# Optimization experiments

Hardware: AMD Instinct MI355X
Metric: run time of the kernel (lower is better)

The kernel has to match this reference:

```python
import jax, jax.numpy as jnp
import numpy as np

# ctlib options layout: [views, dets, width, height, dImg, dDet, Ang0, dAng, s2r, d2r, binshift]
VIEWS = 512
DETS = 512
H_IMG = 256
W_IMG = 256
D_IMG = 0.006641
D_DET = 0.0072
ANG0 = 0.0
D_ANG = 2.0 * np.pi / VIEWS
S2R = 5.95
D2R = 4.906
VIRDET = D_DET * S2R / (S2R + D2R)  # virtual detector spacing at isocenter


def make_filter():
    # ramp (Ram-Lak) filter in spatial domain, length 2*dets-1
    x = np.arange(2 * DETS - 1) - DETS + 1
    x2 = np.where(x == 0, 1, x * x).astype(np.float64)
    f = np.where(np.abs(x) % 2 == 1, -1.0 / (np.pi ** 2 * x2 * VIRDET ** 2), 0.0)
    f = np.where(x == 0, 1.0 / (4.0 * VIRDET ** 2), f)
    return jnp.asarray(f, dtype=jnp.float32).reshape(1, 1, 1, -1)


def make_w():
    # cosine (distance) pre-weight * quadrature step (virdet * pi / views)
    u = (np.arange(DETS) - DETS / 2 + 0.5) * VIRDET
    w = S2R / np.sqrt(S2R ** 2 + u ** 2) * VIRDET * np.pi / VIEWS
    return jnp.asarray(w, dtype=jnp.float32).reshape(1, 1, 1, -1)


def setup_inputs() -> dict:
    key = jax.random.key(0)
    projection = jax.random.normal(key, (2, 1, VIEWS, DETS), dtype=jnp.float32)
    return {"projection": projection, "w": make_w(), "filt": make_filter()}


def ramp_filter(p, filt):
    # p: [B,1,V,D], filt: [1,1,1,2D-1] -> [B,1,V,D] (same padding along detector axis)
    return jax.lax.conv_general_dilated(
        p, filt, window_strides=(1, 1),
        padding=((0, 0), (DETS - 1, DETS - 1)),
        dimension_numbers=("NCHW", "OIHW", "NCHW"))


def backproject_sv(p):
    # pixel-driven equidistant fan-beam backprojection, one output channel per view
    # p: [B,1,V,D] -> [B,V,H,W]
    p3 = p[:, 0]  # [B,V,D]
    betas = ANG0 + D_ANG * jnp.arange(VIEWS, dtype=jnp.float32)
    cb = jnp.cos(betas)[:, None, None]  # [V,1,1]
    sb = jnp.sin(betas)[:, None, None]
    xs = ((jnp.arange(W_IMG, dtype=jnp.float32) - (W_IMG - 1) / 2.0) * D_IMG)[None, None, :]
    ys = (((H_IMG - 1) / 2.0 - jnp.arange(H_IMG, dtype=jnp.float32)) * D_IMG)[None, :, None]
    d = S2R - (xs * cb + ys * sb)               # [V,H,W] source-to-pixel depth
    u = S2R * (ys * cb - xs * sb) / d           # virtual-detector coordinate
    wgt = (S2R / d) ** 2                        # fan-beam U^{-2} weight
    t = u / VIRDET + (DETS - 1) / 2.0           # fractional detector index
    i0 = jnp.floor(t).astype(jnp.int32)
    frac = t - i0
    v0 = (i0 >= 0) & (i0 < DETS)
    v1 = (i0 + 1 >= 0) & (i0 + 1 < DETS)
    i0c = jnp.clip(i0, 0, DETS - 1)
    i1c = jnp.clip(i0 + 1, 0, DETS - 1)
    gather = jax.vmap(lambda pv, idx: pv[:, idx], in_axes=(1, 0), out_axes=1)
    vals0 = gather(p3, i0c)  # [B,V,H,W]
    vals1 = gather(p3, i1c)
    w0 = ((1.0 - frac) * v0)[None]
    w1 = (frac * v1)[None]
    return wgt[None] * (vals0 * w0 + vals1 * w1)


def reference(projection, w, filt):
    p = projection * w                 # per-detector ramp pre-weight
    p = ramp_filter(p, filt)           # full-width ramp convolution
    return backproject_sv(p)           # per-view backprojection [B,V,H,W]
```

## Files before the change

### kernel.cpp

```cpp
#include <hip/hip_runtime.h>
#include <math.h>

#define VIEWS 512
#define DETS  512

typedef float f32x4 __attribute__((ext_vector_type(4)));
typedef float f32x2 __attribute__((ext_vector_type(2)));

constexpr double S2R_D    = 5.95;
constexpr double D2R_D    = 4.906;
constexpr double DDET_D   = 0.0072;
constexpr double VIRDET_D = DDET_D * S2R_D / (S2R_D + D2R_D);
constexpr double DANG_D   = 2.0 * 3.14159265358979323846 / (double)VIEWS;
constexpr double DIMG_D   = 0.006641;

__global__ __launch_bounds__(512, 4) void fbp_fused_kernel(
    const float* __restrict__ proj, const float* __restrict__ wq,
    const float* __restrict__ filt, float* __restrict__ out)
{
    __shared__ __align__(16) float pwpad[2][1536];
    __shared__ __align__(16) float sfe[520];
    __shared__ __align__(16) float rows01[1536];

    const int tid = threadIdx.x;
    const int v   = blockIdx.x;

    const float beta = (float)DANG_D * (float)v;
    const float cb = cosf(beta);
    const float sb = sinf(beta);

    {
        const f32x4 z = {0.f, 0.f, 0.f, 0.f};
        f32x4* pz = (f32x4*)&pwpad[0][0];
        pz[tid] = z;
        if (tid < 256) pz[512 + tid] = z;
        f32x4* rz = (f32x4*)rows01;
        if (tid < 384) rz[tid] = z;
        for (int i = tid; i < 520; i += 512)
            sfe[i] = (i < 512) ? filt[2*i] : 0.0f;
    }
    __syncthreads();

    if (tid < 256) {
        const int rl  = tid >> 7;
        const int t2  = tid & 127;
        const int row = rl * VIEWS + v;
        const f32x4 p4 = *(const f32x4*)(proj + ((size_t)row << 9) + 4*t2);
        const f32x4 w4 = *(const f32x4*)(wq + 4*t2);
        pwpad[rl][511 + 4*t2 + 0] = p4.x * w4.x;
        pwpad[rl][511 + 4*t2 + 1] = p4.y * w4.y;
        pwpad[rl][511 + 4*t2 + 2] = p4.z * w4.z;
        pwpad[rl][511 + 4*t2 + 3] = p4.w * w4.w;
    }
    __syncthreads();

    const int lane = tid & 63;
    const int warp = tid >> 6;

    if (warp < 4) {
        const int rl2 = warp >> 1;
        const int wv  = warp & 1;
        const int d0  = 256*wv + 4*lane;
        const float* P = &pwpad[rl2][0];
        const int e_lo = wv ? 0 : 124;
        const int G    = wv ? 48 : 49;
        const float c0 = filt[511];
        float a0=0.f, a1=0.f, a2=0.f, a3=0.f;
        for (int g = 0; g < G; ++g) {
            const int e0 = e_lo + 8*g;
            const f32x4 S0 = *(const f32x4*)&sfe[e0];
            const f32x4 S1 = *(const f32x4*)&sfe[e0 + 4];
            const float* Pb = P + d0 + 2*e0;
            const f32x4 q0 = *(const f32x4*)(Pb + 0);
            const f32x4 q1 = *(const f32x4*)(Pb + 4);
            const f32x4 q2 = *(const f32x4*)(Pb + 8);
            const f32x4 q3 = *(const f32x4*)(Pb + 12);
            const f32x4 q4 = *(const f32x4*)(Pb + 16);
            const float p[20] = {q0.x,q0.y,q0.z,q0.w, q1.x,q1.y,q1.z,q1.w,
                                 q2.x,q2.y,q2.z,q2.w, q3.x,q3.y,q3.z,q3.w,
                                 q4.x,q4.y,q4.z,q4.w};
            const float s[8]  = {S0.x,S0.y,S0.z,S0.w, S1.x,S1.y,S1.z,S1.w};
            #pragma unroll
            for (int j = 0; j < 8; ++j) {
                a0 = fmaf(p[2*j + 0], s[j], a0);
                a1 = fmaf(p[2*j + 1], s[j], a1);
                a2 = fmaf(p[2*j + 2], s[j], a2);
                a3 = fmaf(p[2*j + 3], s[j], a3);
            }
        }
        a0 = fmaf(P[511 + d0 + 0], c0, a0);
        a1 = fmaf(P[511 + d0 + 1], c0, a1);
        a2 = fmaf(P[511 + d0 + 2], c0, a2);
        a3 = fmaf(P[511 + d0 + 3], c0, a3);
        float* W = &rows01[((128 + d0) << 1) + rl2];
        W[0] = a0; W[2] = a1; W[4] = a2; W[6] = a3;
    }
    __syncthreads();

    {
        const float D    = (float)DIMG_D;
        const float Kf   = (float)(S2R_D / VIRDET_D);
        const int   xi   = 4*lane;
        const float xs0  = ((float)xi - 127.5f) * D;
        const float xc0  = xs0 * cb;
        const float xsbK = (xs0 * sb) * Kf;
        const float dcb  = D * cb;
        const float dsbK = (D * sb) * Kf;
        const float d0c  = 5.95f - xc0;
        const float ysw  = (127.5f - (float)warp) * D;
        const f32x2* R2  = (const f32x2*)rows01;
        f32x4* o0p = (f32x4*)(out + ((size_t)v << 16));
        f32x4* o1p = o0p + 8388608u;

        #pragma unroll 2
        for (int i = 0; i < 32; ++i) {
            const float ys  = fmaf((float)i, -8.0f*D, ysw);
            const float ysb = ys * sb;
            const float ycb = ys * cb;
            const float dbase = d0c - ysb;
            const float nbase = fmaf(Kf, ycb, -xsbK);
            f32x4 o0, o1;
            #pragma unroll
            for (int j = 0; j < 4; ++j) {
                const float jf  = (float)j;
                const float den = fmaf(jf, -dcb,  dbase);
                const float num = fmaf(jf, -dsbK, nbase);
                float inv = __builtin_amdgcn_rcpf(den);
                inv = inv * fmaf(-den, inv, 2.0f);
                const float wgt = 35.4025f * (inv * inv);
                const float t   = fmaf(num, inv, 383.5f);
                const float ft  = floorf(t);
                const float fr  = t - ft;
                const int   idx = (int)ft;
                const f32x2 ab  = R2[idx];
                const f32x2 cd  = R2[idx + 1];
                o0[j] = wgt * fmaf(fr, cd.x - ab.x, ab.x);
                o1[j] = wgt * fmaf(fr, cd.y - ab.y, ab.y);
            }
            const int y = 8*i + warp;
            const size_t p4i = ((size_t)y << 6) + (size_t)lane;
            __builtin_nontemporal_store(o0, o0p + p4i);
            __builtin_nontemporal_store(o1, o1p + p4i);
        }
    }
}

extern "C" void kernel_launch(void* const* d_in, const int* in_sizes, int n_in,
                              void* d_out, int out_size, void* d_ws, size_t ws_size,
                              hipStream_t stream) {
    const float* proj = (const float*)d_in[0];
    const float* wq   = (const float*)d_in[1];
    const float* filt = (const float*)d_in[2];
    float* out = (float*)d_out;
    (void)in_sizes; (void)n_in; (void)out_size; (void)d_ws; (void)ws_size;

    hipLaunchKernelGGL(fbp_fused_kernel, dim3(VIEWS), dim3(512), 0, stream,
                       proj, wq, filt, out);
}
```

Before: 279.4 us.

## Use planar filtered rows and lane-contiguous pixel mapping in backprojection

Replaces the interleaved two-batch filtered-row buffer with two planar rows, so the convolution writes vectorized float4 stores. The backprojection now assigns consecutive lanes to consecutive pixels (stride 64 per j) instead of four adjacent pixels per lane, which should make neighbouring lanes' LDS gather addresses closer and reduce bank conflicts. The cost is that output stores drop from float4 to scalar nontemporal stores and each pixel needs four scalar LDS loads instead of two float2 loads.

Result: no change. 278.5 us (-0.3%).

```diff
diff --git a/kernel.cpp b/kernel.cpp
--- a/kernel.cpp
+++ b/kernel.cpp
@@ -5,7 +5,6 @@
 #define DETS  512
 
 typedef float f32x4 __attribute__((ext_vector_type(4)));
-typedef float f32x2 __attribute__((ext_vector_type(2)));
 
 constexpr double S2R_D    = 5.95;
 constexpr double D2R_D    = 4.906;
@@ -20,7 +19,7 @@
 {
     __shared__ __align__(16) float pwpad[2][1536];
     __shared__ __align__(16) float sfe[520];
-    __shared__ __align__(16) float rows01[1536];
+    __shared__ __align__(16) float rowsP[2][776];
 
     const int tid = threadIdx.x;
     const int v   = blockIdx.x;
@@ -34,8 +33,8 @@
         f32x4* pz = (f32x4*)&pwpad[0][0];
         pz[tid] = z;
         if (tid < 256) pz[512 + tid] = z;
-        f32x4* rz = (f32x4*)rows01;
-        if (tid < 384) rz[tid] = z;
+        f32x4* rz = (f32x4*)&rowsP[0][0];
+        if (tid < 388) rz[tid] = z;
         for (int i = tid; i < 520; i += 512)
             sfe[i] = (i < 512) ? filt[2*i] : 0.0f;
     }
@@ -92,39 +91,38 @@
         a1 = fmaf(P[511 + d0 + 1], c0, a1);
         a2 = fmaf(P[511 + d0 + 2], c0, a2);
         a3 = fmaf(P[511 + d0 + 3], c0, a3);
-        float* W = &rows01[((128 + d0) << 1) + rl2];
-        W[0] = a0; W[2] = a1; W[4] = a2; W[6] = a3;
+        f32x4 r4; r4.x = a0; r4.y = a1; r4.z = a2; r4.w = a3;
+        *(f32x4*)&rowsP[rl2][128 + d0] = r4;
     }
     __syncthreads();
 
     {
         const float D    = (float)DIMG_D;
         const float Kf   = (float)(S2R_D / VIRDET_D);
-        const int   xi   = 4*lane;
-        const float xs0  = ((float)xi - 127.5f) * D;
+        const float xs0  = ((float)lane - 127.5f) * D;
         const float xc0  = xs0 * cb;
         const float xsbK = (xs0 * sb) * Kf;
-        const float dcb  = D * cb;
-        const float dsbK = (D * sb) * Kf;
+        const float dcb64  = (64.0f * D) * cb;
+        const float dsbK64 = (64.0f * D) * sb * Kf;
         const float d0c  = 5.95f - xc0;
-        const float ysw  = (127.5f - (float)warp) * D;
-        const f32x2* R2  = (const f32x2*)rows01;
-        f32x4* o0p = (f32x4*)(out + ((size_t)v << 16));
-        f32x4* o1p = o0p + 8388608u;
+        const float* rA  = &rowsP[0][0];
+        const float* rB  = &rowsP[1][0];
+        float* outv = out + ((size_t)v << 16);
+        float* outv1 = outv + ((size_t)VIEWS << 16);
 
         #pragma unroll 2
         for (int i = 0; i < 32; ++i) {
-            const float ys  = fmaf((float)i, -8.0f*D, ysw);
+            const int   y   = 8*i + warp;
+            const float ys  = (127.5f - (float)y) * D;
             const float ysb = ys * sb;
             const float ycb = ys * cb;
             const float dbase = d0c - ysb;
             const float nbase = fmaf(Kf, ycb, -xsbK);
-            f32x4 o0, o1;
             #pragma unroll
             for (int j = 0; j < 4; ++j) {
                 const float jf  = (float)j;
-                const float den = fmaf(jf, -dcb,  dbase);
-                const float num = fmaf(jf, -dsbK, nbase);
+                const float den = fmaf(jf, -dcb64,  dbase);
+                const float num = fmaf(jf, -dsbK64, nbase);
                 float inv = __builtin_amdgcn_rcpf(den);
                 inv = inv * fmaf(-den, inv, 2.0f);
                 const float wgt = 35.4025f * (inv * inv);
@@ -132,15 +130,16 @@
                 const float ft  = floorf(t);
                 const float fr  = t - ft;
                 const int   idx = (int)ft;
-                const f32x2 ab  = R2[idx];
-                const f32x2 cd  = R2[idx + 1];
-                o0[j] = wgt * fmaf(fr, cd.x - ab.x, ab.x);
-                o1[j] = wgt * fmaf(fr, cd.y - ab.y, ab.y);
+                const float a0 = rA[idx];
+                const float b0 = rA[idx + 1];
+                const float a1 = rB[idx];
+                const float b1 = rB[idx + 1];
+                const float o0 = wgt * fmaf(fr, b0 - a0, a0);
+                const float o1 = wgt * fmaf(fr, b1 - a1, a1);
+                const size_t off = ((size_t)y << 8) + (size_t)(64*j + lane);
+                __builtin_nontemporal_store(o0, outv  + off);
+                __builtin_nontemporal_store(o1, outv1 + off);
             }
-            const int y = 8*i + warp;
-            const size_t p4i = ((size_t)y << 6) + (size_t)lane;
-            __builtin_nontemporal_store(o0, o0p + p4i);
-            __builtin_nontemporal_store(o1, o1p + p4i);
         }
     }
 }
```
